# Kernel tuning notes

Hardware: AMD Instinct MI355X
Metric: run time of the kernel (lower is better)

The kernel has to match this reference:

```python
import jax, jax.numpy as jnp
import numpy as np

K = 24          # num_eigh
D_MODEL = 768   # d_in == d_out
STATE = 100     # LDS state_dim
BSZ = 1
SEQ = 2048


def setup_inputs() -> dict:
    key = jax.random.key(0)
    ks = jax.random.split(key, 8)
    x = jax.random.normal(ks[0], (BSZ, SEQ, D_MODEL), dtype=jnp.float32)
    input_pos = jnp.arange(SEQ, dtype=jnp.int32)
    M_inputs = jax.random.normal(ks[1], (D_MODEL, D_MODEL), dtype=jnp.float32) * 0.02
    M_filters = jax.random.normal(ks[2], (K, D_MODEL), dtype=jnp.float32) * 0.02
    # LDS params: diagonal A (stable, |a|<1), B maps scalar input -> state,
    # C maps state -> 2K outputs, Dv is scalar-input feedthrough to 2K outputs.
    A = jax.random.uniform(ks[3], (STATE,), dtype=jnp.float32, minval=0.0, maxval=0.99)
    Bm = jax.random.normal(ks[4], (STATE,), dtype=jnp.float32) * 0.1
    C = jax.random.normal(ks[5], (STATE, 2 * K), dtype=jnp.float32) * 0.1
    Dv = jax.random.normal(ks[6], (2 * K,), dtype=jnp.float32) * 0.1
    return {"x": x, "input_pos": input_pos, "M_inputs": M_inputs,
            "M_filters": M_filters, "A": A, "Bm": Bm, "C": C, "Dv": Dv}


def reference(x, input_pos, M_inputs, M_filters, A, Bm, C, Dv):
    bsz, seq_len, d_in = x.shape
    k = M_filters.shape[0]
    # input projection (use_approx branch)
    xp = x @ M_inputs                                   # (b, s, d)
    # flatten per-channel scalar sequences: (b*d, s)
    u = xp.transpose(0, 2, 1).reshape(bsz * d_in, seq_len)
    ut = u.T                                            # (s, N) for scan over time
    h0 = jnp.zeros((bsz * d_in, A.shape[0]), dtype=xp.dtype)

    def step(h, u_t):
        # h: (N, state), u_t: (N,) scalar input per lane
        h = h * A[None, :] + u_t[:, None] * Bm[None, :]
        y = h @ C + u_t[:, None] * Dv[None, :]          # (N, 2K)
        return h, y

    _, ys = jax.lax.scan(step, h0, ut)                  # (s, N, 2K)
    # U: (b, s, 2K, d)
    U = ys.transpose(1, 0, 2).reshape(bsz, d_in, seq_len, 2 * k).transpose(0, 2, 3, 1)
    spectral_plus = jnp.einsum('bskd,kd->bsd', U[:, :, k:, :], M_filters)
    spectral_minus = jnp.einsum('bskd,kd->bsd', U[:, :, :k, :], M_filters)
    return spectral_plus + spectral_minus
```

## Files before the change

kernel.cpp:

```cpp
#include <hip/hip_runtime.h>

#define SEQ   2048
#define DM    768
#define ST    100
#define KF    24
#define NC    32
#define KJ    128
#define NJ    112
#define GK2   1536

using short8  = __attribute__((ext_vector_type(8))) short;
using float4v = __attribute__((ext_vector_type(4))) float;

__device__ __forceinline__ unsigned short bf16_rn(float x) {
    unsigned int u = __float_as_uint(x);
    unsigned int r = u + 0x7FFFu + ((u >> 16) & 1u);
    return (unsigned short)(r >> 16);
}
__device__ __forceinline__ float bf2f(unsigned short h) {
    return __uint_as_float(((unsigned int)h) << 16);
}
__device__ __forceinline__ void async16(const void* g, void* l) {
    __builtin_amdgcn_global_load_lds(
        (const __attribute__((address_space(1))) unsigned int*)g,
        (__attribute__((address_space(3))) unsigned int*)l, 16, 0, 0);
}

__global__ __launch_bounds__(256) void prep(const float* __restrict__ x,
                                            const float* __restrict__ Mi,
                                            const float* __restrict__ C,
                                            const float* __restrict__ Dv,
                                            const float* __restrict__ Mf,
                                            const float* __restrict__ Av,
                                            unsigned short* __restrict__ Mbig,
                                            unsigned short* __restrict__ Xbig,
                                            float* __restrict__ WpT,
                                            float* __restrict__ evec,
                                            float* __restrict__ Apow) {
    __shared__ float tl[64][65];
    int bid = blockIdx.x, t = threadIdx.x;
    if (bid < 144) {
        int i0 = (bid / 12) * 64, d0 = (bid % 12) * 64;
        int tx = t & 63, ty = t >> 6;
#pragma unroll
        for (int r = ty; r < 64; r += 4)
            tl[r][tx] = Mi[(i0 + r) * DM + d0 + tx];
        __syncthreads();
#pragma unroll
        for (int r = ty; r < 64; r += 4) {
            float v = tl[tx][r];
            unsigned short h = bf16_rn(v);
            unsigned short lo = bf16_rn(v - bf2f(h));
            unsigned short* row = Mbig + (size_t)(d0 + r) * GK2 + i0 + tx;
            row[0] = h; row[DM] = lo;
        }
    } else if (bid < 912) {
        int idx8 = (bid - 144) * 256 + t;
        int s = idx8 / (DM / 8), i0 = (idx8 % (DM / 8)) * 8;
        const float* xp = x + (size_t)s * DM + i0;
        float4 v0 = *(const float4*)xp;
        float4 v1 = *(const float4*)(xp + 4);
        float av[8] = {v0.x, v0.y, v0.z, v0.w, v1.x, v1.y, v1.z, v1.w};
        short8 hh;
#pragma unroll
        for (int q = 0; q < 8; ++q) hh[q] = (short)bf16_rn(av[q]);
        *(short8*)(Xbig + (size_t)s * DM + i0) = hh;
    } else if (bid < 1212) {
        int tid = (bid - 912) * 256 + t;
        if (tid < ST * DM) {
            int d = tid / ST, j = tid % ST;
            float s = 0.f;
#pragma unroll
            for (int k = 0; k < KF; ++k)
                s += (C[j * 2 * KF + k] + C[j * 2 * KF + KF + k]) * Mf[k * DM + d];
            WpT[tid] = s;
        }
        if (tid < DM) {
            float s = 0.f;
#pragma unroll
            for (int k = 0; k < KF; ++k)
                s += (Dv[k] + Dv[KF + k]) * Mf[k * DM + tid];
            evec[tid] = s;
        }
    } else {
        if (t < ST) {
            float a = Av[t];
            float p = 1.f;
            for (int dlt = 0; dlt <= 64; ++dlt) { Apow[dlt * ST + t] = p; p *= a; }
        }
    }
}

__global__ __launch_bounds__(256) void tables(const float* __restrict__ Bv,
                                              const float* __restrict__ Apow,
                                              const float* __restrict__ WpT,
                                              float* __restrict__ Kmat,
                                              unsigned short* __restrict__ Ehi,
                                              unsigned short* __restrict__ Elo,
                                              unsigned short* __restrict__ Qhi,
                                              unsigned short* __restrict__ Qlo) {
    int tid = blockIdx.x * 256 + threadIdx.x;
    if (tid < 64 * DM) {
        int dlt = tid / DM, d = tid % DM;
        float s = 0.f;
        for (int j = 0; j < ST; ++j)
            s += Bv[j] * Apow[dlt * ST + j] * WpT[d * ST + j];
        Kmat[dlt * DM + d] = s;
    } else if (tid < 64 * DM + 64 * KJ) {
        int r = tid - 64 * DM;
        int tt = r >> 7, j = r & 127;
        float v = (j < ST) ? Apow[(tt + 1) * ST + j] : 0.f;
        unsigned short h = bf16_rn(v);
        unsigned short lo = bf16_rn(v - bf2f(h));
        Ehi[tt * KJ + j] = h;
        Elo[tt * KJ + j] = lo;
    } else {
        int r = tid - 64 * DM - 64 * KJ;
        if (r < NJ * 64) {
            int j = r >> 6, i = r & 63;
            float v = (j < ST) ? Bv[j] * Apow[(63 - i) * ST + j] : 0.f;
            unsigned short h = bf16_rn(v);
            unsigned short lo = bf16_rn(v - bf2f(h));
            Qhi[j * 64 + i] = h;
            Qlo[j * 64 + i] = lo;
        }
    }
}

__global__ __launch_bounds__(256) void gemm_mfma(const unsigned short* __restrict__ Mbig,
                                                 const unsigned short* __restrict__ Xbig,
                                                 float* __restrict__ ut0,
                                                 float* __restrict__ ut1) {
    __shared__ unsigned short As[64 * 32];
    __shared__ unsigned short Bs[64 * 32];
    int t = threadIdx.x;
    int tile = blockIdx.x;
    int d0 = (tile % (DM / 64)) * 64;
    int s0 = (tile / (DM / 64)) * 64;
    int ks = blockIdx.y;
    int kb0 = ks * DM;
    float* utp = ks ? ut1 : ut0;
    int wave = t >> 6, lane = t & 63;
    int m16 = lane & 15, quad = lane >> 4;
    int r0 = t >> 2, q0 = ((t & 3) - (t >> 3)) & 3;
    float4v acc[4];
#pragma unroll
    for (int nt = 0; nt < 4; ++nt) acc[nt] = (float4v){0.f, 0.f, 0.f, 0.f};
    for (int k0 = 0; k0 < DM; k0 += 32) {
        __syncthreads();
        async16(&Mbig[(size_t)(d0 + r0) * GK2 + kb0 + k0 + q0 * 8], &As[(size_t)t * 8]);
        async16(&Xbig[(size_t)(s0 + r0) * DM + k0 + q0 * 8], &Bs[(size_t)t * 8]);
        __syncthreads();
        int arow = wave * 16 + m16;
        int aqp = (quad + (arow >> 1)) & 3;
        short8 af = *(short8*)&As[arow * 32 + aqp * 8];
        short8 bf[4];
#pragma unroll
        for (int nt = 0; nt < 4; ++nt) {
            int brow = nt * 16 + m16;
            int bqp = (quad + (brow >> 1)) & 3;
            bf[nt] = *(short8*)&Bs[brow * 32 + bqp * 8];
        }
#pragma unroll
        for (int nt = 0; nt < 4; ++nt)
            acc[nt] = __builtin_amdgcn_mfma_f32_16x16x32_bf16(af, bf[nt], acc[nt], 0, 0, 0);
    }
#pragma unroll
    for (int nt = 0; nt < 4; ++nt) {
        int dd = d0 + wave * 16 + quad * 4;
        int ss = s0 + nt * 16 + m16;
#pragma unroll
        for (int i = 0; i < 4; ++i)
            utp[(size_t)(dd + i) * SEQ + ss] = acc[nt][i];
    }
}

__global__ __launch_bounds__(256) void hscanG(const float* __restrict__ ut0,
                                              const float* __restrict__ ut1,
                                              const unsigned short* __restrict__ Qhi,
                                              const unsigned short* __restrict__ Qlo,
                                              const float* __restrict__ WpT,
                                              const float* __restrict__ Apow,
                                              unsigned short* __restrict__ Ghi,
                                              unsigned short* __restrict__ Glo) {
    __shared__ float hl[64][120];
    int m0 = blockIdx.x * 64;
    int wave = threadIdx.x >> 6, lane = threadIdx.x & 63;
    int m16 = lane & 15, quad = lane >> 4;
    float4v acc[7];
#pragma unroll
    for (int nt = 0; nt < 7; ++nt) acc[nt] = (float4v){0.f, 0.f, 0.f, 0.f};
#pragma unroll
    for (int ks = 0; ks < 2; ++ks) {
        size_t ao = (size_t)(m0 + wave * 16 + m16) * 64 + ks * 32 + quad * 8;
        float4 a0 = *(const float4*)(ut0 + ao);
        float4 a1 = *(const float4*)(ut0 + ao + 4);
        float4 b0 = *(const float4*)(ut1 + ao);
        float4 b1 = *(const float4*)(ut1 + ao + 4);
        float av[8] = {a0.x + b0.x, a0.y + b0.y, a0.z + b0.z, a0.w + b0.w,
                       a1.x + b1.x, a1.y + b1.y, a1.z + b1.z, a1.w + b1.w};
        short8 ah, al;
#pragma unroll
        for (int q = 0; q < 8; ++q) {
            unsigned short h = bf16_rn(av[q]);
            ah[q] = (short)h;
            al[q] = (short)bf16_rn(av[q] - bf2f(h));
        }
#pragma unroll
        for (int nt = 0; nt < 7; ++nt) {
            int qoff = (nt * 16 + m16) * 64 + ks * 32 + quad * 8;
            short8 bh = *(const short8*)(Qhi + qoff);
            short8 bl = *(const short8*)(Qlo + qoff);
            acc[nt] = __builtin_amdgcn_mfma_f32_16x16x32_bf16(ah, bh, acc[nt], 0, 0, 0);
            acc[nt] = __builtin_amdgcn_mfma_f32_16x16x32_bf16(ah, bl, acc[nt], 0, 0, 0);
            acc[nt] = __builtin_amdgcn_mfma_f32_16x16x32_bf16(al, bh, acc[nt], 0, 0, 0);
        }
    }
#pragma unroll
    for (int nt = 0; nt < 7; ++nt)
#pragma unroll
        for (int i = 0; i < 4; ++i)
            hl[wave * 16 + quad * 4 + i][nt * 16 + m16] = acc[nt][i];
    __syncthreads();

    int j = threadIdx.x & 127, dloc = threadIdx.x >> 7;
    int d = blockIdx.x * 2 + dloc;
    bool ja = (j < ST);
    float a64 = ja ? Apow[64 * ST + j] : 0.f;
    float w   = ja ? WpT[d * ST + j] : 0.f;
    float hs = 0.f;
    for (int c = 0; c < NC; ++c) {
        float g = ja ? (w * hs) : 0.f;
        unsigned short gh = bf16_rn(g);
        unsigned short gl = bf16_rn(g - bf2f(gh));
        size_t go = ((size_t)c * DM + d) * KJ + j;
        Ghi[go] = gh;
        Glo[go] = gl;
        float add = ja ? hl[dloc * 32 + c][j] : 0.f;
        hs = fmaf(a64, hs, add);
    }
}

__global__ __launch_bounds__(64) void intra(const float* __restrict__ ut0,
                                            float* uy,
                                            const float* __restrict__ Kmat,
                                            const float* __restrict__ evec) {
    int lane = threadIdx.x;
    int d = blockIdx.x * 2 + (lane >> 5);
    int c = lane & 31;
    size_t off = (size_t)d * SEQ + c * 64;
    float uu[64];
#pragma unroll
    for (int q = 0; q < 16; ++q) {
        float4 v0 = *(const float4*)(ut0 + off + q * 4);
        float4 v1 = *(const float4*)(uy + off + q * 4);
        uu[q * 4 + 0] = v0.x + v1.x; uu[q * 4 + 1] = v0.y + v1.y;
        uu[q * 4 + 2] = v0.z + v1.z; uu[q * 4 + 3] = v0.w + v1.w;
    }
    float e = evec[d];
    float y[64];
#pragma unroll
    for (int t = 0; t < 64; ++t) y[t] = e * uu[t];
#pragma unroll
    for (int dlt = 0; dlt < 64; ++dlt) {
        float k = Kmat[dlt * DM + d];
#pragma unroll
        for (int t = dlt; t < 64; ++t)
            y[t] = fmaf(k, uu[t - dlt], y[t]);
    }
#pragma unroll
    for (int q = 0; q < 16; ++q) {
        float4 v = make_float4(y[q * 4 + 0], y[q * 4 + 1], y[q * 4 + 2], y[q * 4 + 3]);
        *(float4*)(uy + off + q * 4) = v;
    }
}

__global__ __launch_bounds__(256) void inter(const unsigned short* __restrict__ Ehi,
                                             const unsigned short* __restrict__ Elo,
                                             const unsigned short* __restrict__ Ghi,
                                             const unsigned short* __restrict__ Glo,
                                             const float* __restrict__ yintra,
                                             float* __restrict__ out) {
    __shared__ float yl[64][129];
    int c = blockIdx.x;
    int d0 = blockIdx.y * 128;
    int wave = threadIdx.x >> 6, lane = threadIdx.x & 63;
    int wn = wave * 32;
    int m16 = lane & 15, quad = lane >> 4;
#pragma unroll
    for (int it = 0; it < 8; ++it) {
        int idx = threadIdx.x + it * 256;
        int row = idx >> 4, col4 = (idx & 15) * 4;
        float4 v = *(const float4*)&yintra[(size_t)(d0 + row) * SEQ + c * 64 + col4];
        yl[col4 + 0][row] = v.x;
        yl[col4 + 1][row] = v.y;
        yl[col4 + 2][row] = v.z;
        yl[col4 + 3][row] = v.w;
    }
    float4v acc[4][2];
#pragma unroll
    for (int mt = 0; mt < 4; ++mt)
#pragma unroll
        for (int nt = 0; nt < 2; ++nt) acc[mt][nt] = (float4v){0.f, 0.f, 0.f, 0.f};
#pragma unroll
    for (int ks = 0; ks < 4; ++ks) {
        short8 bh[2], bl[2];
#pragma unroll
        for (int nt = 0; nt < 2; ++nt) {
            size_t ga = ((size_t)c * DM + d0 + wn + nt * 16 + m16) * KJ + ks * 32 + quad * 8;
            bh[nt] = *(const short8*)(Ghi + ga);
            bl[nt] = *(const short8*)(Glo + ga);
        }
#pragma unroll
        for (int mt = 0; mt < 4; ++mt) {
            int eo = (mt * 16 + m16) * KJ + ks * 32 + quad * 8;
            short8 ah = *(const short8*)(Ehi + eo);
            short8 al = *(const short8*)(Elo + eo);
#pragma unroll
            for (int nt = 0; nt < 2; ++nt) {
                acc[mt][nt] = __builtin_amdgcn_mfma_f32_16x16x32_bf16(ah, bh[nt], acc[mt][nt], 0, 0, 0);
                acc[mt][nt] = __builtin_amdgcn_mfma_f32_16x16x32_bf16(ah, bl[nt], acc[mt][nt], 0, 0, 0);
                acc[mt][nt] = __builtin_amdgcn_mfma_f32_16x16x32_bf16(al, bh[nt], acc[mt][nt], 0, 0, 0);
            }
        }
    }
    __syncthreads();
#pragma unroll
    for (int mt = 0; mt < 4; ++mt)
#pragma unroll
        for (int nt = 0; nt < 2; ++nt) {
            int tt = mt * 16 + quad * 4;
            int dcol = wn + nt * 16 + m16;
#pragma unroll
            for (int i = 0; i < 4; ++i) {
                float v = acc[mt][nt][i] + yl[tt + i][dcol];
                out[(size_t)(c * 64 + tt + i) * DM + d0 + dcol] = v;
            }
        }
}

extern "C" void kernel_launch(void* const* d_in, const int* in_sizes, int n_in,
                              void* d_out, int out_size, void* d_ws, size_t ws_size,
                              hipStream_t stream) {
    const float* x  = (const float*)d_in[0];
    const float* Mi = (const float*)d_in[2];
    const float* Mf = (const float*)d_in[3];
    const float* Av = (const float*)d_in[4];
    const float* Bv = (const float*)d_in[5];
    const float* C  = (const float*)d_in[6];
    const float* Dv = (const float*)d_in[7];
    float* out = (float*)d_out;

    float* ut0    = (float*)d_ws;
    float* WpT    = ut0 + (size_t)DM * SEQ;
    float* ev     = WpT + DM * ST;
    float* Apow   = ev + DM;
    float* Kmat   = Apow + 65 * ST;
    float* ut1    = Kmat + 64 * DM;
    unsigned short* Mbig = (unsigned short*)(ut1 + (size_t)DM * SEQ);
    unsigned short* Xbig = Mbig + (size_t)DM * GK2;
    unsigned short* Ehi  = Xbig + (size_t)SEQ * DM;
    unsigned short* Elo  = Ehi + 64 * KJ;
    unsigned short* Qhi  = Elo + 64 * KJ;
    unsigned short* Qlo  = Qhi + NJ * 64;
    unsigned short* Ghi  = Qlo + NJ * 64;
    unsigned short* Glo  = Ghi + (size_t)NC * DM * KJ;

    prep<<<1213, 256, 0, stream>>>(x, Mi, C, Dv, Mf, Av, Mbig, Xbig, WpT, ev, Apow);
    tables<<<252, 256, 0, stream>>>(Bv, Apow, WpT, Kmat, Ehi, Elo, Qhi, Qlo);
    gemm_mfma<<<dim3((DM / 64) * (SEQ / 64), 2), 256, 0, stream>>>(Mbig, Xbig, ut0, ut1);
    hscanG<<<384, 256, 0, stream>>>(ut0, ut1, Qhi, Qlo, WpT, Apow, Ghi, Glo);
    intra<<<384, 64, 0, stream>>>(ut0, ut1, Kmat, ev);
    inter<<<dim3(NC, DM / 128), 256, 0, stream>>>(Ehi, Elo, Ghi, Glo, ut1, out);
}
```

Baseline: 138.7 us.

## Fuse table build into prep, merge scan with intra conv, retile inter

Moves the Apow/E/Q table generation into the prep kernel and computes the per-delta convolution taps inside the scan kernel, eliminating the separate tables kernel and Kmat buffer. The chunk-state scan and the intra-chunk convolution are fused into one kernel so that ut1 is read and overwritten by the same block, removing a launch. The inter kernel is retiled to 64 output columns per block to double the grid. This trades launch overhead and an intermediate buffer for serialized intra work within each fused block and redundant tap computation per block.

```diff
diff --git a/kernel.cpp b/kernel.cpp
--- a/kernel.cpp
+++ b/kernel.cpp
@@ -32,11 +32,16 @@
                                             const float* __restrict__ Dv,
                                             const float* __restrict__ Mf,
                                             const float* __restrict__ Av,
+                                            const float* __restrict__ Bv,
                                             unsigned short* __restrict__ Mbig,
                                             unsigned short* __restrict__ Xbig,
                                             float* __restrict__ WpT,
                                             float* __restrict__ evec,
-                                            float* __restrict__ Apow) {
+                                            float* __restrict__ Apow,
+                                            unsigned short* __restrict__ Ehi,
+                                            unsigned short* __restrict__ Elo,
+                                            unsigned short* __restrict__ Qhi,
+                                            unsigned short* __restrict__ Qlo) {
     __shared__ float tl[64][65];
     int bid = blockIdx.x, t = threadIdx.x;
     if (bid < 144) {
@@ -83,46 +88,25 @@
             evec[tid] = s;
         }
     } else {
-        if (t < ST) {
-            float a = Av[t];
+        if (t < KJ) {
+            bool ja = (t < ST);
+            float a = ja ? Av[t] : 0.f;
+            float b = ja ? Bv[t] : 0.f;
             float p = 1.f;
-            for (int dlt = 0; dlt <= 64; ++dlt) { Apow[dlt * ST + t] = p; p *= a; }
-        }
-    }
-}
-
-__global__ __launch_bounds__(256) void tables(const float* __restrict__ Bv,
-                                              const float* __restrict__ Apow,
-                                              const float* __restrict__ WpT,
-                                              float* __restrict__ Kmat,
-                                              unsigned short* __restrict__ Ehi,
-                                              unsigned short* __restrict__ Elo,
-                                              unsigned short* __restrict__ Qhi,
-                                              unsigned short* __restrict__ Qlo) {
-    int tid = blockIdx.x * 256 + threadIdx.x;
-    if (tid < 64 * DM) {
-        int dlt = tid / DM, d = tid % DM;
-        float s = 0.f;
-        for (int j = 0; j < ST; ++j)
-            s += Bv[j] * Apow[dlt * ST + j] * WpT[d * ST + j];
-        Kmat[dlt * DM + d] = s;
-    } else if (tid < 64 * DM + 64 * KJ) {
-        int r = tid - 64 * DM;
-        int tt = r >> 7, j = r & 127;
-        float v = (j < ST) ? Apow[(tt + 1) * ST + j] : 0.f;
-        unsigned short h = bf16_rn(v);
-        unsigned short lo = bf16_rn(v - bf2f(h));
-        Ehi[tt * KJ + j] = h;
-        Elo[tt * KJ + j] = lo;
-    } else {
-        int r = tid - 64 * DM - 64 * KJ;
-        if (r < NJ * 64) {
-            int j = r >> 6, i = r & 63;
-            float v = (j < ST) ? Bv[j] * Apow[(63 - i) * ST + j] : 0.f;
-            unsigned short h = bf16_rn(v);
-            unsigned short lo = bf16_rn(v - bf2f(h));
-            Qhi[j * 64 + i] = h;
-            Qlo[j * 64 + i] = lo;
+            for (int dlt = 0; dlt < 64; ++dlt) {
+                if (ja) Apow[dlt * ST + t] = p;
+                if (t < NJ) {
+                    float v = b * p;
+                    unsigned short h = bf16_rn(v);
+                    Qhi[t * 64 + 63 - dlt] = h;
+                    Qlo[t * 64 + 63 - dlt] = bf16_rn(v - bf2f(h));
+                }
+                p *= a;
+                unsigned short h = bf16_rn(p);
+                Ehi[dlt * KJ + t] = h;
+                Elo[dlt * KJ + t] = bf16_rn(p - bf2f(h));
+            }
+            if (ja) Apow[64 * ST + t] = p;
         }
     }
 }
@@ -175,103 +159,115 @@
     }
 }
 
-__global__ __launch_bounds__(256) void hscanG(const float* __restrict__ ut0,
-                                              const float* __restrict__ ut1,
-                                              const unsigned short* __restrict__ Qhi,
-                                              const unsigned short* __restrict__ Qlo,
-                                              const float* __restrict__ WpT,
-                                              const float* __restrict__ Apow,
-                                              unsigned short* __restrict__ Ghi,
-                                              unsigned short* __restrict__ Glo) {
+__global__ __launch_bounds__(256) void scanf_k(const float* __restrict__ ut0,
+                                               float* uy,
+                                               const unsigned short* __restrict__ Qhi,
+                                               const unsigned short* __restrict__ Qlo,
+                                               const float* __restrict__ WpT,
+                                               const float* __restrict__ Apow,
+                                               const float* __restrict__ Bv,
+                                               const float* __restrict__ evec,
+                                               unsigned short* __restrict__ Ghi,
+                                               unsigned short* __restrict__ Glo) {
     __shared__ float hl[64][120];
+    __shared__ float kk[128];
+    int t = threadIdx.x;
     int m0 = blockIdx.x * 64;
-    int wave = threadIdx.x >> 6, lane = threadIdx.x & 63;
+    int d0 = blockIdx.x * 2;
+    if (t < 128) {
+        int dlt = t & 63, dloc = t >> 6;
+        const float* wrow = WpT + (d0 + dloc) * ST;
+        float s = 0.f;
+        for (int j = 0; j < ST; ++j)
+            s = fmaf(Bv[j] * Apow[dlt * ST + j], wrow[j], s);
+        kk[t] = s;
+    }
+    int wave = t >> 6, lane = t & 63;
     int m16 = lane & 15, quad = lane >> 4;
-    float4v acc[7];
-#pragma unroll
-    for (int nt = 0; nt < 7; ++nt) acc[nt] = (float4v){0.f, 0.f, 0.f, 0.f};
-#pragma unroll
-    for (int ks = 0; ks < 2; ++ks) {
-        size_t ao = (size_t)(m0 + wave * 16 + m16) * 64 + ks * 32 + quad * 8;
-        float4 a0 = *(const float4*)(ut0 + ao);
-        float4 a1 = *(const float4*)(ut0 + ao + 4);
-        float4 b0 = *(const float4*)(ut1 + ao);
-        float4 b1 = *(const float4*)(ut1 + ao + 4);
-        float av[8] = {a0.x + b0.x, a0.y + b0.y, a0.z + b0.z, a0.w + b0.w,
-                       a1.x + b1.x, a1.y + b1.y, a1.z + b1.z, a1.w + b1.w};
-        short8 ah, al;
-#pragma unroll
-        for (int q = 0; q < 8; ++q) {
-            unsigned short h = bf16_rn(av[q]);
-            ah[q] = (short)h;
-            al[q] = (short)bf16_rn(av[q] - bf2f(h));
-        }
-#pragma unroll
-        for (int nt = 0; nt < 7; ++nt) {
-            int qoff = (nt * 16 + m16) * 64 + ks * 32 + quad * 8;
-            short8 bh = *(const short8*)(Qhi + qoff);
-            short8 bl = *(const short8*)(Qlo + qoff);
-            acc[nt] = __builtin_amdgcn_mfma_f32_16x16x32_bf16(ah, bh, acc[nt], 0, 0, 0);
-            acc[nt] = __builtin_amdgcn_mfma_f32_16x16x32_bf16(ah, bl, acc[nt], 0, 0, 0);
-            acc[nt] = __builtin_amdgcn_mfma_f32_16x16x32_bf16(al, bh, acc[nt], 0, 0, 0);
-        }
-    }
-#pragma unroll
-    for (int nt = 0; nt < 7; ++nt)
-#pragma unroll
-        for (int i = 0; i < 4; ++i)
-            hl[wave * 16 + quad * 4 + i][nt * 16 + m16] = acc[nt][i];
+    {
+        float4v acc[7];
+#pragma unroll
+        for (int nt = 0; nt < 7; ++nt) acc[nt] = (float4v){0.f, 0.f, 0.f, 0.f};
+#pragma unroll
+        for (int ks = 0; ks < 2; ++ks) {
+            size_t ao = (size_t)(m0 + wave * 16 + m16) * 64 + ks * 32 + quad * 8;
+            float4 a0 = *(const float4*)(ut0 + ao);
+            float4 a1 = *(const float4*)(ut0 + ao + 4);
+            float4 b0 = *(const float4*)(uy + ao);
+            float4 b1 = *(const float4*)(uy + ao + 4);
+            float av[8] = {a0.x + b0.x, a0.y + b0.y, a0.z + b0.z, a0.w + b0.w,
+                           a1.x + b1.x, a1.y + b1.y, a1.z + b1.z, a1.w + b1.w};
+            short8 ah, al;
+#pragma unroll
+            for (int q = 0; q < 8; ++q) {
+                unsigned short h = bf16_rn(av[q]);
+                ah[q] = (short)h;
+                al[q] = (short)bf16_rn(av[q] - bf2f(h));
+            }
+#pragma unroll
+            for (int nt = 0; nt < 7; ++nt) {
+                int qoff = (nt * 16 + m16) * 64 + ks * 32 + quad * 8;
+                short8 bh = *(const short8*)(Qhi + qoff);
+                short8 bl = *(const short8*)(Qlo + qoff);
+                acc[nt] = __builtin_amdgcn_mfma_f32_16x16x32_bf16(ah, bh, acc[nt], 0, 0, 0);
+                acc[nt] = __builtin_amdgcn_mfma_f32_16x16x32_bf16(ah, bl, acc[nt], 0, 0, 0);
+                acc[nt] = __builtin_amdgcn_mfma_f32_16x16x32_bf16(al, bh, acc[nt], 0, 0, 0);
+            }
+        }
+#pragma unroll
+        for (int nt = 0; nt < 7; ++nt)
+#pragma unroll
+            for (int i = 0; i < 4; ++i)
+                hl[wave * 16 + quad * 4 + i][nt * 16 + m16] = acc[nt][i];
+    }
     __syncthreads();
-
-    int j = threadIdx.x & 127, dloc = threadIdx.x >> 7;
-    int d = blockIdx.x * 2 + dloc;
-    bool ja = (j < ST);
-    float a64 = ja ? Apow[64 * ST + j] : 0.f;
-    float w   = ja ? WpT[d * ST + j] : 0.f;
-    float hs = 0.f;
-    for (int c = 0; c < NC; ++c) {
-        float g = ja ? (w * hs) : 0.f;
-        unsigned short gh = bf16_rn(g);
-        unsigned short gl = bf16_rn(g - bf2f(gh));
-        size_t go = ((size_t)c * DM + d) * KJ + j;
-        Ghi[go] = gh;
-        Glo[go] = gl;
-        float add = ja ? hl[dloc * 32 + c][j] : 0.f;
-        hs = fmaf(a64, hs, add);
-    }
-}
-
-__global__ __launch_bounds__(64) void intra(const float* __restrict__ ut0,
-                                            float* uy,
-                                            const float* __restrict__ Kmat,
-                                            const float* __restrict__ evec) {
-    int lane = threadIdx.x;
-    int d = blockIdx.x * 2 + (lane >> 5);
-    int c = lane & 31;
-    size_t off = (size_t)d * SEQ + c * 64;
-    float uu[64];
-#pragma unroll
-    for (int q = 0; q < 16; ++q) {
-        float4 v0 = *(const float4*)(ut0 + off + q * 4);
-        float4 v1 = *(const float4*)(uy + off + q * 4);
-        uu[q * 4 + 0] = v0.x + v1.x; uu[q * 4 + 1] = v0.y + v1.y;
-        uu[q * 4 + 2] = v0.z + v1.z; uu[q * 4 + 3] = v0.w + v1.w;
-    }
-    float e = evec[d];
-    float y[64];
-#pragma unroll
-    for (int t = 0; t < 64; ++t) y[t] = e * uu[t];
-#pragma unroll
-    for (int dlt = 0; dlt < 64; ++dlt) {
-        float k = Kmat[dlt * DM + d];
-#pragma unroll
-        for (int t = dlt; t < 64; ++t)
-            y[t] = fmaf(k, uu[t - dlt], y[t]);
-    }
-#pragma unroll
-    for (int q = 0; q < 16; ++q) {
-        float4 v = make_float4(y[q * 4 + 0], y[q * 4 + 1], y[q * 4 + 2], y[q * 4 + 3]);
-        *(float4*)(uy + off + q * 4) = v;
+    {
+        int j = t & 127, dloc = t >> 7;
+        int d = d0 + dloc;
+        bool ja = (j < ST);
+        float a64 = ja ? Apow[64 * ST + j] : 0.f;
+        float w   = ja ? WpT[d * ST + j] : 0.f;
+        float hs = 0.f;
+        for (int c = 0; c < NC; ++c) {
+            float g = ja ? (w * hs) : 0.f;
+            unsigned short gh = bf16_rn(g);
+            unsigned short gl = bf16_rn(g - bf2f(gh));
+            size_t go = ((size_t)c * DM + d) * KJ + j;
+            Ghi[go] = gh;
+            Glo[go] = gl;
+            float add = ja ? hl[dloc * 32 + c][j] : 0.f;
+            hs = fmaf(a64, hs, add);
+        }
+    }
+    if (t < 64) {
+        int dloc = t >> 5, c = t & 31;
+        int d = d0 + dloc;
+        size_t off = (size_t)d * SEQ + c * 64;
+        float uu[64];
+#pragma unroll
+        for (int q = 0; q < 16; ++q) {
+            float4 v0 = *(const float4*)(ut0 + off + q * 4);
+            float4 v1 = *(const float4*)(uy + off + q * 4);
+            uu[q * 4 + 0] = v0.x + v1.x; uu[q * 4 + 1] = v0.y + v1.y;
+            uu[q * 4 + 2] = v0.z + v1.z; uu[q * 4 + 3] = v0.w + v1.w;
+        }
+        float e = evec[d];
+        float y[64];
+#pragma unroll
+        for (int tt = 0; tt < 64; ++tt) y[tt] = e * uu[tt];
+        const float* kt = &kk[dloc * 64];
+#pragma unroll
+        for (int dlt = 0; dlt < 64; ++dlt) {
+            float k = kt[dlt];
+#pragma unroll
+            for (int tt = dlt; tt < 64; ++tt)
+                y[tt] = fmaf(k, uu[tt - dlt], y[tt]);
+        }
+#pragma unroll
+        for (int q = 0; q < 16; ++q) {
+            float4 v = make_float4(y[q * 4 + 0], y[q * 4 + 1], y[q * 4 + 2], y[q * 4 + 3]);
+            *(float4*)(uy + off + q * 4) = v;
+        }
     }
 }
 
@@ -281,15 +277,13 @@
                                              const unsigned short* __restrict__ Glo,
                                              const float* __restrict__ yintra,
                                              float* __restrict__ out) {
-    __shared__ float yl[64][129];
+    __shared__ float yl[64][68];
     int c = blockIdx.x;
-    int d0 = blockIdx.y * 128;
-    int wave = threadIdx.x >> 6, lane = threadIdx.x & 63;
-    int wn = wave * 32;
-    int m16 = lane & 15, quad = lane >> 4;
-#pragma unroll
-    for (int it = 0; it < 8; ++it) {
-        int idx = threadIdx.x + it * 256;
+    int d0 = blockIdx.y * 64;
+    int t = threadIdx.x;
+#pragma unroll
+    for (int it = 0; it < 4; ++it) {
+        int idx = t + it * 256;
         int row = idx >> 4, col4 = (idx & 15) * 4;
         float4 v = *(const float4*)&yintra[(size_t)(d0 + row) * SEQ + c * 64 + col4];
         yl[col4 + 0][row] = v.x;
@@ -297,46 +291,38 @@
         yl[col4 + 2][row] = v.z;
         yl[col4 + 3][row] = v.w;
     }
-    float4v acc[4][2];
-#pragma unroll
-    for (int mt = 0; mt < 4; ++mt)
-#pragma unroll
-        for (int nt = 0; nt < 2; ++nt) acc[mt][nt] = (float4v){0.f, 0.f, 0.f, 0.f};
+    __syncthreads();
+    int wave = t >> 6, lane = t & 63;
+    int wn = wave * 16;
+    int m16 = lane & 15, quad = lane >> 4;
+    float4v acc[4];
+#pragma unroll
+    for (int mt = 0; mt < 4; ++mt) acc[mt] = (float4v){0.f, 0.f, 0.f, 0.f};
 #pragma unroll
     for (int ks = 0; ks < 4; ++ks) {
-        short8 bh[2], bl[2];
-#pragma unroll
-        for (int nt = 0; nt < 2; ++nt) {
-            size_t ga = ((size_t)c * DM + d0 + wn + nt * 16 + m16) * KJ + ks * 32 + quad * 8;
-            bh[nt] = *(const short8*)(Ghi + ga);
-            bl[nt] = *(const short8*)(Glo + ga);
-        }
+        size_t gb = ((size_t)c * DM + d0 + wn + m16) * KJ + ks * 32 + quad * 8;
+        short8 bh = *(const short8*)(Ghi + gb);
+        short8 bl = *(const short8*)(Glo + gb);
 #pragma unroll
         for (int mt = 0; mt < 4; ++mt) {
             int eo = (mt * 16 + m16) * KJ + ks * 32 + quad * 8;
             short8 ah = *(const short8*)(Ehi + eo);
             short8 al = *(const short8*)(Elo + eo);
-#pragma unroll
-            for (int nt = 0; nt < 2; ++nt) {
-                acc[mt][nt] = __builtin_amdgcn_mfma_f32_16x16x32_bf16(ah, bh[nt], acc[mt][nt], 0, 0, 0);
-                acc[mt][nt] = __builtin_amdgcn_mfma_f32_16x16x32_bf16(ah, bl[nt], acc[mt][nt], 0, 0, 0);
-                acc[mt][nt] = __builtin_amdgcn_mfma_f32_16x16x32_bf16(al, bh[nt], acc[mt][nt], 0, 0, 0);
-            }
-        }
-    }
-    __syncthreads();
-#pragma unroll
-    for (int mt = 0; mt < 4; ++mt)
-#pragma unroll
-        for (int nt = 0; nt < 2; ++nt) {
-            int tt = mt * 16 + quad * 4;
-            int dcol = wn + nt * 16 + m16;
-#pragma unroll
-            for (int i = 0; i < 4; ++i) {
-                float v = acc[mt][nt][i] + yl[tt + i][dcol];
-                out[(size_t)(c * 64 + tt + i) * DM + d0 + dcol] = v;
-            }
-        }
+            acc[mt] = __builtin_amdgcn_mfma_f32_16x16x32_bf16(ah, bh, acc[mt], 0, 0, 0);
+            acc[mt] = __builtin_amdgcn_mfma_f32_16x16x32_bf16(ah, bl, acc[mt], 0, 0, 0);
+            acc[mt] = __builtin_amdgcn_mfma_f32_16x16x32_bf16(al, bh, acc[mt], 0, 0, 0);
+        }
+    }
+#pragma unroll
+    for (int mt = 0; mt < 4; ++mt) {
+        int tt = mt * 16 + quad * 4;
+        int dcol = wn + m16;
+#pragma unroll
+        for (int i = 0; i < 4; ++i) {
+            float v = acc[mt][i] + yl[tt + i][dcol];
+            out[(size_t)(c * 64 + tt + i) * DM + d0 + dcol] = v;
+        }
+    }
 }
 
 extern "C" void kernel_launch(void* const* d_in, const int* in_sizes, int n_in,
@@ -355,8 +341,7 @@
     float* WpT    = ut0 + (size_t)DM * SEQ;
     float* ev     = WpT + DM * ST;
     float* Apow   = ev + DM;
-    float* Kmat   = Apow + 65 * ST;
-    float* ut1    = Kmat + 64 * DM;
+    float* ut1    = Apow + 65 * ST;
     unsigned short* Mbig = (unsigned short*)(ut1 + (size_t)DM * SEQ);
     unsigned short* Xbig = Mbig + (size_t)DM * GK2;
     unsigned short* Ehi  = Xbig + (size_t)SEQ * DM;
@@ -366,10 +351,9 @@
     unsigned short* Ghi  = Qlo + NJ * 64;
     unsigned short* Glo  = Ghi + (size_t)NC * DM * KJ;
 
-    prep<<<1213, 256, 0, stream>>>(x, Mi, C, Dv, Mf, Av, Mbig, Xbig, WpT, ev, Apow);
-    tables<<<252, 256, 0, stream>>>(Bv, Apow, WpT, Kmat, Ehi, Elo, Qhi, Qlo);
+    prep<<<1213, 256, 0, stream>>>(x, Mi, C, Dv, Mf, Av, Bv, Mbig, Xbig,
+                                   WpT, ev, Apow, Ehi, Elo, Qhi, Qlo);
     gemm_mfma<<<dim3((DM / 64) * (SEQ / 64), 2), 256, 0, stream>>>(Mbig, Xbig, ut0, ut1);
-    hscanG<<<384, 256, 0, stream>>>(ut0, ut1, Qhi, Qlo, WpT, Apow, Ghi, Glo);
-    intra<<<384, 64, 0, stream>>>(ut0, ut1, Kmat, ev);
-    inter<<<dim3(NC, DM / 128), 256, 0, stream>>>(Ehi, Elo, Ghi, Glo, ut1, out);
-}
+    scanf_k<<<384, 256, 0, stream>>>(ut0, ut1, Qhi, Qlo, WpT, Apow, Bv, ev, Ghi, Glo);
+    inter<<<dim3(NC, DM / 64), 256, 0, stream>>>(Ehi, Elo, Ghi, Glo, ut1, out);
+}
```

Result: no change. 137.4 us (-1.0%).
